# Kernel optimization log

Measured on AMD Instinct MI355X. Metric: run time of the kernel, lower is better.

## Reference

```python
import jax, jax.numpy as jnp
import numpy as np

GROUPS = 8

def conv1d(x, w, b, stride=1, groups=1):
    # x: [B,C,L], w: [O, I//groups, K]
    y = jax.lax.conv_general_dilated(x, w, (stride,), 'VALID',
        dimension_numbers=('NCH', 'OIH', 'NCH'), feature_group_count=groups)
    return y + b[None, :, None]

def shuffle1d(x, groups):
    B, C, L = x.shape
    cpg = C // groups
    return x.reshape(B, groups, cpg, L).transpose(0, 2, 1, 3).reshape(B, C, L)

def setup_inputs() -> dict:
    key = jax.random.key(0)
    ks = jax.random.split(key, 12)
    C = 256
    B, L = 8, 4096
    g = GROUPS
    sc = 0.05
    inp = {
        'x':   jax.random.normal(ks[0], (B, C, L), dtype=jnp.float32),
        'w1':  jax.random.normal(ks[1], (C, C // g, 3), dtype=jnp.float32) * sc,
        'b1':  jax.random.normal(ks[2], (C,), dtype=jnp.float32) * sc,
        'w2':  jax.random.normal(ks[3], (C, C // g, 3), dtype=jnp.float32) * sc,
        'b2':  jax.random.normal(ks[4], (C,), dtype=jnp.float32) * sc,
        'wa1': jax.random.normal(ks[5], (C, 2 * C // g, 1), dtype=jnp.float32) * sc,
        'ba1': jax.random.normal(ks[6], (C,), dtype=jnp.float32) * sc,
        'wa2': jax.random.normal(ks[7], (C, C // g, 1), dtype=jnp.float32) * sc,
        'ba2': jax.random.normal(ks[8], (C,), dtype=jnp.float32) * sc,
        'w3':  jax.random.normal(ks[9], (C, C // g, 5), dtype=jnp.float32) * sc,  # kernel_size-4=5
        'b3':  jax.random.normal(ks[10], (C,), dtype=jnp.float32) * sc,
    }
    return inp

def reference(x, w1, b1, w2, b2, wa1, ba1, wa2, ba2, w3, b3):
    g = GROUPS
    # in_state has length 0 at init, so cat is identity; L >= kernel_size.
    h = conv1d(x, w1, b1, stride=1, groups=g)      # [B,C,L-2]
    h = shuffle1d(h, g)
    h = conv1d(h, w2, b2, stride=1, groups=g)      # [B,C,L-4]
    h = shuffle1d(h, g)
    # SortAttn: stable ascending sort over channel dim
    sorted_h = jnp.sort(h, axis=1, stable=True)
    a = conv1d(jnp.concatenate((sorted_h, h), axis=1), wa1, ba1, stride=1, groups=g)
    a = shuffle1d(a, g)
    a = jax.nn.sigmoid(conv1d(a, wa2, ba2, stride=1, groups=g))
    h = h * a
    y = conv1d(h, w3, b3, stride=1, groups=g)      # [B,C,L-8]
    return y
```

## Files before the change

### kernel.cpp

```cpp
#include <hip/hip_runtime.h>
#include <math.h>

#define BB 8
#define CCH 256
#define LLEN 4096
#define L1V 4094
#define L2V 4092
#define L3V 4088
#define NCOL (BB * L2V)

__global__ void prep_kernel(const float* __restrict__ wa1, const float* __restrict__ wa2,
                            float* __restrict__ wt1T, float* __restrict__ wt2T) {
    int i = blockIdx.x;
    int o = threadIdx.x;
    if (i < 64) {
        wt1T[i * 256 + o] = wa1[o * 64 + i];
    } else {
        int ii = i - 64;
        if (ii < 32) wt2T[ii * 256 + o] = wa2[o * 32 + ii];
    }
}

__global__ __launch_bounds__(256) void conv1_kernel(const float* __restrict__ x,
                                                    const float* __restrict__ w1,
                                                    const float* __restrict__ b1,
                                                    float* __restrict__ t1) {
    __shared__ float xs[9248];
    const int b = blockIdx.y;
    const int l0 = blockIdx.x * 32;
    const int t = threadIdx.x;

#pragma unroll
    for (int j = 0; j < 9; ++j) {
        int f = t + 256 * j;
        int row = f / 9;
        int q = f - row * 9;
        size_t rb = (size_t)(b * CCH + row) * LLEN;
        float4 v;
        int base = l0 + 4 * q;
        if (base + 3 < LLEN) {
            v = *(const float4*)(x + rb + base);
        } else {
            v.x = x[rb + min(base + 0, LLEN - 1)];
            v.y = x[rb + min(base + 1, LLEN - 1)];
            v.z = x[rb + min(base + 2, LLEN - 1)];
            v.w = x[rb + min(base + 3, LLEN - 1)];
        }
        int a = row * 36 + (row >> 5) * 4 + 4 * q;
        *(float4*)&xs[a] = v;
    }
    __syncthreads();

    const int oc = t;
    const int go = t >> 5;
    float acc[32];
#pragma unroll
    for (int l = 0; l < 32; ++l) acc[l] = 0.f;

    for (int i = 0; i < 32; ++i) {
        int row = go * 32 + i;
        int base = row * 36 + go * 4;
        float rw[36];
#pragma unroll
        for (int q = 0; q < 9; ++q) *(float4*)&rw[4 * q] = *(const float4*)&xs[base + 4 * q];
        float wv0 = w1[oc * 96 + i * 3 + 0];
        float wv1 = w1[oc * 96 + i * 3 + 1];
        float wv2 = w1[oc * 96 + i * 3 + 2];
#pragma unroll
        for (int l = 0; l < 32; ++l) acc[l] += wv0 * rw[l] + wv1 * rw[l + 1] + wv2 * rw[l + 2];
    }
    float bias = b1[oc];
    int nc = (oc & 31) * 8 + (oc >> 5);
    float* dst = t1 + (size_t)(b * L1V + l0) * CCH + nc;
#pragma unroll
    for (int l = 0; l < 32; ++l) {
        if (l0 + l < L1V) dst[(size_t)l * CCH] = acc[l] + bias;
    }
}

__global__ __launch_bounds__(256) void conv2_kernel(const float* __restrict__ t1,
                                                    const float* __restrict__ w2,
                                                    const float* __restrict__ b2,
                                                    float* __restrict__ t2) {
    __shared__ float ts[9792];
    const int b = blockIdx.y;
    const int l0 = blockIdx.x * 32;
    const int t = threadIdx.x;

#pragma unroll
    for (int j = 0; j < 9; ++j) {
        int f = t + 256 * j;
        if (f < 2176) {
            int p = f >> 6;
            int c4 = (f & 63) * 4;
            int row = min(l0 + p, L1V - 1);
            float4 v = *(const float4*)(t1 + (size_t)(b * L1V + row) * CCH + c4);
            *(float4*)&ts[p * 288 + (c4 >> 5) * 36 + (c4 & 31)] = v;
        }
    }
    __syncthreads();

    const int oc = t;
    const int go = t >> 5;
    float acc[32];
#pragma unroll
    for (int l = 0; l < 32; ++l) acc[l] = 0.f;

    for (int i4 = 0; i4 < 8; ++i4) {
        float wv[12];
#pragma unroll
        for (int z = 0; z < 12; ++z) wv[z] = w2[oc * 96 + i4 * 12 + z];
        int colbase = go * 36 + i4 * 4;
#pragma unroll
        for (int p = 0; p < 34; ++p) {
            float4 rv = *(const float4*)&ts[p * 288 + colbase];
#pragma unroll
            for (int cc = 0; cc < 4; ++cc) {
                float xv = (&rv.x)[cc];
#pragma unroll
                for (int k = 0; k < 3; ++k) {
                    int l = p - k;
                    if (l >= 0 && l < 32) acc[l] += wv[cc * 3 + k] * xv;
                }
            }
        }
    }
    float bias = b2[oc];
    int nc = (oc & 31) * 8 + (oc >> 5);
    float* dst = t2 + (size_t)(b * L2V + l0) * CCH + nc;
#pragma unroll
    for (int l = 0; l < 32; ++l) {
        if (l0 + l < L2V) dst[(size_t)l * CCH] = acc[l] + bias;
    }
}

__device__ __forceinline__ void ce_pair(float& a, float& b, bool up) {
    float lo = fminf(a, b), hi = fmaxf(a, b);
    a = up ? lo : hi;
    b = up ? hi : lo;
}

__device__ __forceinline__ void bitonic256(float v[4], int lane) {
#pragma unroll
    for (int k = 2; k <= 256; k <<= 1) {
#pragma unroll
        for (int j = k >> 1; j > 0; j >>= 1) {
            if (j >= 4) {
                int lm = j >> 2;
                bool upper = (lane & lm) != 0;
#pragma unroll
                for (int r = 0; r < 4; ++r) {
                    float other = __shfl_xor(v[r], lm, 64);
                    bool dirUp = (((4 * lane + r) & k) == 0);
                    bool keepMin = (dirUp != upper);
                    float lo = fminf(v[r], other), hi = fmaxf(v[r], other);
                    v[r] = keepMin ? lo : hi;
                }
            } else if (j == 2) {
#pragma unroll
                for (int r = 0; r < 2; ++r) {
                    bool up = (((4 * lane + r) & k) == 0);
                    ce_pair(v[r], v[r + 2], up);
                }
            } else {
#pragma unroll
                for (int r = 0; r < 4; r += 2) {
                    bool up = (((4 * lane + r) & k) == 0);
                    ce_pair(v[r], v[r + 1], up);
                }
            }
        }
    }
}

__global__ __launch_bounds__(256) void attn_kernel(float* __restrict__ t2,
                                                   const float* __restrict__ wt1T,
                                                   const float* __restrict__ wt2T,
                                                   const float* __restrict__ ba1,
                                                   const float* __restrict__ ba2) {
    __shared__ float sm[13440];
    const int t = threadIdx.x;
    const int wv = t >> 6;
    const int lane = t & 63;
    const int wbase = wv * 3360;
    const int go = lane >> 3;

    float4 ba1v = *(const float4*)&ba1[4 * lane];
    float4 ba2v = *(const float4*)&ba2[4 * lane];

    for (int pass = 0; pass < 4; ++pass) {
        int colBase = blockIdx.x * 64 + wv * 16 + pass * 4;

        float4 hv[4];
#pragma unroll
        for (int cc = 0; cc < 4; ++cc) {
            int col = colBase + cc;
            if (col < NCOL) hv[cc] = *(const float4*)(t2 + (size_t)col * CCH + 4 * lane);
            else hv[cc] = make_float4(0.f, 0.f, 0.f, 0.f);
        }
#pragma unroll
        for (int r = 0; r < 4; ++r) {
            int e = 4 * lane + r;
            int slot = ((e >> 6) + 4) * 65 + (e & 63);
            float4 vvv = make_float4((&hv[0].x)[r], (&hv[1].x)[r], (&hv[2].x)[r], (&hv[3].x)[r]);
            *(float4*)&sm[wbase + slot * 4] = vvv;
        }
        float srt[4][4];
#pragma unroll
        for (int cc = 0; cc < 4; ++cc) {
            float s[4] = {hv[cc].x, hv[cc].y, hv[cc].z, hv[cc].w};
            bitonic256(s, lane);
            srt[cc][0] = s[0]; srt[cc][1] = s[1]; srt[cc][2] = s[2]; srt[cc][3] = s[3];
        }
#pragma unroll
        for (int r = 0; r < 4; ++r) {
            int e = 4 * lane + r;
            int slot = (e >> 6) * 65 + (e & 63);
            float4 vvv = make_float4(srt[0][r], srt[1][r], srt[2][r], srt[3][r]);
            *(float4*)&sm[wbase + slot * 4] = vvv;
        }
        __syncthreads();

        float4 acc[4];
#pragma unroll
        for (int cc = 0; cc < 4; ++cc) acc[cc] = make_float4(0.f, 0.f, 0.f, 0.f);
#pragma unroll 4
        for (int i = 0; i < 64; ++i) {
            float4 w4 = *(const float4*)&wt1T[i * 256 + 4 * lane];
            float4 cv = *(const float4*)&sm[wbase + (go * 65 + i) * 4];
#pragma unroll
            for (int cc = 0; cc < 4; ++cc) {
                float cvv = (&cv.x)[cc];
                acc[cc].x += w4.x * cvv;
                acc[cc].y += w4.y * cvv;
                acc[cc].z += w4.z * cvv;
                acc[cc].w += w4.w * cvv;
            }
        }
#pragma unroll
        for (int r = 0; r < 4; ++r) {
            float bb = (&ba1v.x)[r];
            float4 vvv = make_float4((&acc[0].x)[r] + bb, (&acc[1].x)[r] + bb,
                                     (&acc[2].x)[r] + bb, (&acc[3].x)[r] + bb);
            *(float4*)&sm[wbase + 2080 + (5 * lane + r) * 4] = vvv;
        }
        __syncthreads();

        float4 acc2[4];
#pragma unroll
        for (int cc = 0; cc < 4; ++cc) acc2[cc] = make_float4(0.f, 0.f, 0.f, 0.f);
#pragma unroll 4
        for (int i = 0; i < 32; ++i) {
            float4 w4 = *(const float4*)&wt2T[i * 256 + 4 * lane];
            int idx = ((i & 7) << 5) + (go << 2) + (i >> 3);
            int slotA = idx + (idx >> 2);
            float4 av = *(const float4*)&sm[wbase + 2080 + slotA * 4];
#pragma unroll
            for (int cc = 0; cc < 4; ++cc) {
                float avv = (&av.x)[cc];
                acc2[cc].x += w4.x * avv;
                acc2[cc].y += w4.y * avv;
                acc2[cc].z += w4.z * avv;
                acc2[cc].w += w4.w * avv;
            }
        }
#pragma unroll
        for (int cc = 0; cc < 4; ++cc) {
            int col = colBase + cc;
            if (col < NCOL) {
                float zx = acc2[cc].x + ba2v.x;
                float zy = acc2[cc].y + ba2v.y;
                float zz = acc2[cc].z + ba2v.z;
                float zw = acc2[cc].w + ba2v.w;
                float4 res;
                res.x = hv[cc].x * (1.f / (1.f + __expf(-zx)));
                res.y = hv[cc].y * (1.f / (1.f + __expf(-zy)));
                res.z = hv[cc].z * (1.f / (1.f + __expf(-zz)));
                res.w = hv[cc].w * (1.f / (1.f + __expf(-zw)));
                *(float4*)(t2 + (size_t)col * CCH + 4 * lane) = res;
            }
        }
    }
}

__global__ __launch_bounds__(256) void conv3_kernel(const float* __restrict__ hm,
                                                    const float* __restrict__ w3,
                                                    const float* __restrict__ b3,
                                                    float* __restrict__ out) {
    __shared__ float ts[10368];
    const int b = blockIdx.y;
    const int l0 = blockIdx.x * 32;
    const int t = threadIdx.x;

#pragma unroll
    for (int j = 0; j < 9; ++j) {
        int f = t + 256 * j;
        int p = f >> 6;
        int c4 = (f & 63) * 4;
        int row = min(l0 + p, L2V - 1);
        float4 v = *(const float4*)(hm + (size_t)(b * L2V + row) * CCH + c4);
        *(float4*)&ts[p * 288 + (c4 >> 5) * 36 + (c4 & 31)] = v;
    }
    __syncthreads();

    const int oc = t;
    const int go = t >> 5;
    float acc[32];
#pragma unroll
    for (int l = 0; l < 32; ++l) acc[l] = 0.f;

    for (int i4 = 0; i4 < 8; ++i4) {
        float wv[20];
#pragma unroll
        for (int z = 0; z < 20; ++z) wv[z] = w3[oc * 160 + i4 * 20 + z];
        int colbase = go * 36 + i4 * 4;
#pragma unroll
        for (int p = 0; p < 36; ++p) {
            float4 rv = *(const float4*)&ts[p * 288 + colbase];
#pragma unroll
            for (int cc = 0; cc < 4; ++cc) {
                float xv = (&rv.x)[cc];
#pragma unroll
                for (int k = 0; k < 5; ++k) {
                    int l = p - k;
                    if (l >= 0 && l < 32) acc[l] += wv[cc * 5 + k] * xv;
                }
            }
        }
    }
    float bias = b3[oc];
    float* dst = out + (size_t)(b * CCH + oc) * L3V + l0;
#pragma unroll
    for (int l4 = 0; l4 < 8; ++l4) {
        int gl = l0 + 4 * l4;
        if (gl + 3 < L3V) {
            float4 v;
            v.x = acc[4 * l4 + 0] + bias;
            v.y = acc[4 * l4 + 1] + bias;
            v.z = acc[4 * l4 + 2] + bias;
            v.w = acc[4 * l4 + 3] + bias;
            *(float4*)(dst + 4 * l4) = v;
        } else {
#pragma unroll
            for (int c = 0; c < 4; ++c) {
                if (gl + c < L3V) dst[4 * l4 + c] = acc[4 * l4 + c] + bias;
            }
        }
    }
}

extern "C" void kernel_launch(void* const* d_in, const int* in_sizes, int n_in,
                              void* d_out, int out_size, void* d_ws, size_t ws_size,
                              hipStream_t stream) {
    const float* x   = (const float*)d_in[0];
    const float* w1  = (const float*)d_in[1];
    const float* b1  = (const float*)d_in[2];
    const float* w2  = (const float*)d_in[3];
    const float* b2  = (const float*)d_in[4];
    const float* wa1 = (const float*)d_in[5];
    const float* ba1 = (const float*)d_in[6];
    const float* wa2 = (const float*)d_in[7];
    const float* ba2 = (const float*)d_in[8];
    const float* w3  = (const float*)d_in[9];
    const float* b3  = (const float*)d_in[10];
    float* out = (float*)d_out;

    char* ws = (char*)d_ws;
    float* t1   = (float*)ws;
    float* t2   = (float*)(ws + ((size_t)32 << 20));
    float* wt1T = (float*)(ws + ((size_t)64 << 20));
    float* wt2T = wt1T + 64 * 256;

    hipLaunchKernelGGL(prep_kernel, dim3(96), dim3(256), 0, stream, wa1, wa2, wt1T, wt2T);
    hipLaunchKernelGGL(conv1_kernel, dim3(128, BB), dim3(256), 0, stream, x, w1, b1, t1);
    hipLaunchKernelGGL(conv2_kernel, dim3(128, BB), dim3(256), 0, stream, t1, w2, b2, t2);
    hipLaunchKernelGGL(attn_kernel, dim3(512), dim3(256), 0, stream, t2, wt1T, wt2T, ba1, ba2);
    hipLaunchKernelGGL(conv3_kernel, dim3(128, BB), dim3(256), 0, stream, t2, w3, b3, out);
}
```

Baseline: 321.0 us.

## Raise occupancy: launch bounds, streamed conv1 loads, one-pass attention blocks

Adds a minimum of 4 blocks per CU to the launch bounds of all conv and attention kernels. The conv1 inner loop now consumes shared-memory float4 loads directly into the accumulators instead of staging a 36-float register row. The attention kernel drops its 4-pass loop and the __syncthreads (each wave uses only its own shared-memory slice), reuses one shared buffer per wave for both stages, and launches 2046 blocks of 16 columns each. The aim is lower register and LDS pressure and more waves in flight, at the risk of spills under the tighter register cap and of dropping the column bounds check, which relies on NCOL dividing exactly by 16.

```diff
diff --git a/kernel.cpp b/kernel.cpp
--- a/kernel.cpp
+++ b/kernel.cpp
@@ -21,10 +21,10 @@
     }
 }
 
-__global__ __launch_bounds__(256) void conv1_kernel(const float* __restrict__ x,
-                                                    const float* __restrict__ w1,
-                                                    const float* __restrict__ b1,
-                                                    float* __restrict__ t1) {
+__global__ __launch_bounds__(256, 4) void conv1_kernel(const float* __restrict__ x,
+                                                       const float* __restrict__ w1,
+                                                       const float* __restrict__ b1,
+                                                       float* __restrict__ t1) {
     __shared__ float xs[9248];
     const int b = blockIdx.y;
     const int l0 = blockIdx.x * 32;
@@ -60,14 +60,21 @@
     for (int i = 0; i < 32; ++i) {
         int row = go * 32 + i;
         int base = row * 36 + go * 4;
-        float rw[36];
-#pragma unroll
-        for (int q = 0; q < 9; ++q) *(float4*)&rw[4 * q] = *(const float4*)&xs[base + 4 * q];
         float wv0 = w1[oc * 96 + i * 3 + 0];
         float wv1 = w1[oc * 96 + i * 3 + 1];
         float wv2 = w1[oc * 96 + i * 3 + 2];
 #pragma unroll
-        for (int l = 0; l < 32; ++l) acc[l] += wv0 * rw[l] + wv1 * rw[l + 1] + wv2 * rw[l + 2];
+        for (int q = 0; q < 9; ++q) {
+            float4 v = *(const float4*)&xs[base + 4 * q];
+#pragma unroll
+            for (int j = 0; j < 4; ++j) {
+                int e = 4 * q + j;
+                float xv = (&v.x)[j];
+                if (e < 32) acc[e] += wv0 * xv;
+                if (e >= 1 && e <= 32) acc[e - 1] += wv1 * xv;
+                if (e >= 2 && e <= 33) acc[e - 2] += wv2 * xv;
+            }
+        }
     }
     float bias = b1[oc];
     int nc = (oc & 31) * 8 + (oc >> 5);
@@ -78,10 +85,10 @@
     }
 }
 
-__global__ __launch_bounds__(256) void conv2_kernel(const float* __restrict__ t1,
-                                                    const float* __restrict__ w2,
-                                                    const float* __restrict__ b2,
-                                                    float* __restrict__ t2) {
+__global__ __launch_bounds__(256, 4) void conv2_kernel(const float* __restrict__ t1,
+                                                       const float* __restrict__ w2,
+                                                       const float* __restrict__ b2,
+                                                       float* __restrict__ t2) {
     __shared__ float ts[9792];
     const int b = blockIdx.y;
     const int l0 = blockIdx.x * 32;
@@ -173,120 +180,111 @@
     }
 }
 
-__global__ __launch_bounds__(256) void attn_kernel(float* __restrict__ t2,
-                                                   const float* __restrict__ wt1T,
-                                                   const float* __restrict__ wt2T,
-                                                   const float* __restrict__ ba1,
-                                                   const float* __restrict__ ba2) {
-    __shared__ float sm[13440];
+__global__ __launch_bounds__(256, 4) void attn_kernel(float* __restrict__ t2,
+                                                      const float* __restrict__ wt1T,
+                                                      const float* __restrict__ wt2T,
+                                                      const float* __restrict__ ba1,
+                                                      const float* __restrict__ ba2) {
+    __shared__ float sm[8320];
     const int t = threadIdx.x;
     const int wv = t >> 6;
     const int lane = t & 63;
-    const int wbase = wv * 3360;
+    const int wbase = wv * 2080;
     const int go = lane >> 3;
 
     float4 ba1v = *(const float4*)&ba1[4 * lane];
     float4 ba2v = *(const float4*)&ba2[4 * lane];
 
-    for (int pass = 0; pass < 4; ++pass) {
-        int colBase = blockIdx.x * 64 + wv * 16 + pass * 4;
-
-        float4 hv[4];
+    const int colBase = blockIdx.x * 16 + wv * 4;
+
+    float4 hv[4];
+#pragma unroll
+    for (int cc = 0; cc < 4; ++cc) {
+        hv[cc] = *(const float4*)(t2 + (size_t)(colBase + cc) * CCH + 4 * lane);
+    }
+#pragma unroll
+    for (int r = 0; r < 4; ++r) {
+        int e = 4 * lane + r;
+        int slot = ((e >> 6) + 4) * 65 + (e & 63);
+        float4 vvv = make_float4((&hv[0].x)[r], (&hv[1].x)[r], (&hv[2].x)[r], (&hv[3].x)[r]);
+        *(float4*)&sm[wbase + slot * 4] = vvv;
+    }
+    float srt[4][4];
+#pragma unroll
+    for (int cc = 0; cc < 4; ++cc) {
+        float s[4] = {hv[cc].x, hv[cc].y, hv[cc].z, hv[cc].w};
+        bitonic256(s, lane);
+        srt[cc][0] = s[0]; srt[cc][1] = s[1]; srt[cc][2] = s[2]; srt[cc][3] = s[3];
+    }
+#pragma unroll
+    for (int r = 0; r < 4; ++r) {
+        int e = 4 * lane + r;
+        int slot = (e >> 6) * 65 + (e & 63);
+        float4 vvv = make_float4(srt[0][r], srt[1][r], srt[2][r], srt[3][r]);
+        *(float4*)&sm[wbase + slot * 4] = vvv;
+    }
+
+    float4 acc[4];
+#pragma unroll
+    for (int cc = 0; cc < 4; ++cc) acc[cc] = make_float4(0.f, 0.f, 0.f, 0.f);
+#pragma unroll 4
+    for (int i = 0; i < 64; ++i) {
+        float4 w4 = *(const float4*)&wt1T[i * 256 + 4 * lane];
+        float4 cv = *(const float4*)&sm[wbase + (go * 65 + i) * 4];
 #pragma unroll
         for (int cc = 0; cc < 4; ++cc) {
-            int col = colBase + cc;
-            if (col < NCOL) hv[cc] = *(const float4*)(t2 + (size_t)col * CCH + 4 * lane);
-            else hv[cc] = make_float4(0.f, 0.f, 0.f, 0.f);
-        }
-#pragma unroll
-        for (int r = 0; r < 4; ++r) {
-            int e = 4 * lane + r;
-            int slot = ((e >> 6) + 4) * 65 + (e & 63);
-            float4 vvv = make_float4((&hv[0].x)[r], (&hv[1].x)[r], (&hv[2].x)[r], (&hv[3].x)[r]);
-            *(float4*)&sm[wbase + slot * 4] = vvv;
-        }
-        float srt[4][4];
+            float cvv = (&cv.x)[cc];
+            acc[cc].x += w4.x * cvv;
+            acc[cc].y += w4.y * cvv;
+            acc[cc].z += w4.z * cvv;
+            acc[cc].w += w4.w * cvv;
+        }
+    }
+#pragma unroll
+    for (int r = 0; r < 4; ++r) {
+        float bb = (&ba1v.x)[r];
+        float4 vvv = make_float4((&acc[0].x)[r] + bb, (&acc[1].x)[r] + bb,
+                                 (&acc[2].x)[r] + bb, (&acc[3].x)[r] + bb);
+        *(float4*)&sm[wbase + (5 * lane + r) * 4] = vvv;
+    }
+
+    float4 acc2[4];
+#pragma unroll
+    for (int cc = 0; cc < 4; ++cc) acc2[cc] = make_float4(0.f, 0.f, 0.f, 0.f);
+#pragma unroll 4
+    for (int i = 0; i < 32; ++i) {
+        float4 w4 = *(const float4*)&wt2T[i * 256 + 4 * lane];
+        int idx = ((i & 7) << 5) + (go << 2) + (i >> 3);
+        int slotA = idx + (idx >> 2);
+        float4 av = *(const float4*)&sm[wbase + slotA * 4];
 #pragma unroll
         for (int cc = 0; cc < 4; ++cc) {
-            float s[4] = {hv[cc].x, hv[cc].y, hv[cc].z, hv[cc].w};
-            bitonic256(s, lane);
-            srt[cc][0] = s[0]; srt[cc][1] = s[1]; srt[cc][2] = s[2]; srt[cc][3] = s[3];
-        }
-#pragma unroll
-        for (int r = 0; r < 4; ++r) {
-            int e = 4 * lane + r;
-            int slot = (e >> 6) * 65 + (e & 63);
-            float4 vvv = make_float4(srt[0][r], srt[1][r], srt[2][r], srt[3][r]);
-            *(float4*)&sm[wbase + slot * 4] = vvv;
-        }
-        __syncthreads();
-
-        float4 acc[4];
-#pragma unroll
-        for (int cc = 0; cc < 4; ++cc) acc[cc] = make_float4(0.f, 0.f, 0.f, 0.f);
-#pragma unroll 4
-        for (int i = 0; i < 64; ++i) {
-            float4 w4 = *(const float4*)&wt1T[i * 256 + 4 * lane];
-            float4 cv = *(const float4*)&sm[wbase + (go * 65 + i) * 4];
-#pragma unroll
-            for (int cc = 0; cc < 4; ++cc) {
-                float cvv = (&cv.x)[cc];
-                acc[cc].x += w4.x * cvv;
-                acc[cc].y += w4.y * cvv;
-                acc[cc].z += w4.z * cvv;
-                acc[cc].w += w4.w * cvv;
-            }
-        }
-#pragma unroll
-        for (int r = 0; r < 4; ++r) {
-            float bb = (&ba1v.x)[r];
-            float4 vvv = make_float4((&acc[0].x)[r] + bb, (&acc[1].x)[r] + bb,
-                                     (&acc[2].x)[r] + bb, (&acc[3].x)[r] + bb);
-            *(float4*)&sm[wbase + 2080 + (5 * lane + r) * 4] = vvv;
-        }
-        __syncthreads();
-
-        float4 acc2[4];
-#pragma unroll
-        for (int cc = 0; cc < 4; ++cc) acc2[cc] = make_float4(0.f, 0.f, 0.f, 0.f);
-#pragma unroll 4
-        for (int i = 0; i < 32; ++i) {
-            float4 w4 = *(const float4*)&wt2T[i * 256 + 4 * lane];
-            int idx = ((i & 7) << 5) + (go << 2) + (i >> 3);
-            int slotA = idx + (idx >> 2);
-            float4 av = *(const float4*)&sm[wbase + 2080 + slotA * 4];
-#pragma unroll
-            for (int cc = 0; cc < 4; ++cc) {
-                float avv = (&av.x)[cc];
-                acc2[cc].x += w4.x * avv;
-                acc2[cc].y += w4.y * avv;
-                acc2[cc].z += w4.z * avv;
-                acc2[cc].w += w4.w * avv;
-            }
-        }
-#pragma unroll
-        for (int cc = 0; cc < 4; ++cc) {
-            int col = colBase + cc;
-            if (col < NCOL) {
-                float zx = acc2[cc].x + ba2v.x;
-                float zy = acc2[cc].y + ba2v.y;
-                float zz = acc2[cc].z + ba2v.z;
-                float zw = acc2[cc].w + ba2v.w;
-                float4 res;
-                res.x = hv[cc].x * (1.f / (1.f + __expf(-zx)));
-                res.y = hv[cc].y * (1.f / (1.f + __expf(-zy)));
-                res.z = hv[cc].z * (1.f / (1.f + __expf(-zz)));
-                res.w = hv[cc].w * (1.f / (1.f + __expf(-zw)));
-                *(float4*)(t2 + (size_t)col * CCH + 4 * lane) = res;
-            }
-        }
-    }
-}
-
-__global__ __launch_bounds__(256) void conv3_kernel(const float* __restrict__ hm,
-                                                    const float* __restrict__ w3,
-                                                    const float* __restrict__ b3,
-                                                    float* __restrict__ out) {
+            float avv = (&av.x)[cc];
+            acc2[cc].x += w4.x * avv;
+            acc2[cc].y += w4.y * avv;
+            acc2[cc].z += w4.z * avv;
+            acc2[cc].w += w4.w * avv;
+        }
+    }
+#pragma unroll
+    for (int cc = 0; cc < 4; ++cc) {
+        float zx = acc2[cc].x + ba2v.x;
+        float zy = acc2[cc].y + ba2v.y;
+        float zz = acc2[cc].z + ba2v.z;
+        float zw = acc2[cc].w + ba2v.w;
+        float4 res;
+        res.x = hv[cc].x * (1.f / (1.f + __expf(-zx)));
+        res.y = hv[cc].y * (1.f / (1.f + __expf(-zy)));
+        res.z = hv[cc].z * (1.f / (1.f + __expf(-zz)));
+        res.w = hv[cc].w * (1.f / (1.f + __expf(-zw)));
+        *(float4*)(t2 + (size_t)(colBase + cc) * CCH + 4 * lane) = res;
+    }
+}
+
+__global__ __launch_bounds__(256, 4) void conv3_kernel(const float* __restrict__ hm,
+                                                       const float* __restrict__ w3,
+                                                       const float* __restrict__ b3,
+                                                       float* __restrict__ out) {
     __shared__ float ts[10368];
     const int b = blockIdx.y;
     const int l0 = blockIdx.x * 32;
@@ -374,6 +372,6 @@
     hipLaunchKernelGGL(prep_kernel, dim3(96), dim3(256), 0, stream, wa1, wa2, wt1T, wt2T);
     hipLaunchKernelGGL(conv1_kernel, dim3(128, BB), dim3(256), 0, stream, x, w1, b1, t1);
     hipLaunchKernelGGL(conv2_kernel, dim3(128, BB), dim3(256), 0, stream, t1, w2, b2, t2);
-    hipLaunchKernelGGL(attn_kernel, dim3(512), dim3(256), 0, stream, t2, wt1T, wt2T, ba1, ba2);
+    hipLaunchKernelGGL(attn_kernel, dim3(2046), dim3(256), 0, stream, t2, wt1T, wt2T, ba1, ba2);
     hipLaunchKernelGGL(conv3_kernel, dim3(128, BB), dim3(256), 0, stream, t2, w3, b3, out);
 }
```

Measured after the change: 298.8 us. 6.9% less time.
